# Kernel tuning notes

Measured on AMD Instinct MI355X. Metric: run time of the kernel, lower is better.

The kernel has to match this reference:

```python
import jax, jax.numpy as jnp
import numpy as np

B, N, DIM, H, DK, DV = 2, 2048, 1536, 8, 64, 192


def relative_shift(x):
    # x: [b, h, t1, 2*t1-1] -> [b, h, t1, t1] via Transformer-XL pad/reshape trick
    b, h, t1, t2 = x.shape
    x = jnp.pad(x, ((0, 0), (0, 0), (0, 0), (1, 0)))  # prepend zero column
    t2p = t2 + 1
    x = x.reshape(b, h, t2p, t1)
    x = x[:, :, 1:, :].reshape(b, h, t1, t2)
    return x[..., : (t2p + 1) // 2]


def setup_inputs() -> dict:
    key = jax.random.key(0)
    ks = jax.random.split(key, 9)
    s = 0.02
    return {
        "x": jax.random.normal(ks[0], (B, N, DIM), jnp.float32),
        "Wq": jax.random.normal(ks[1], (DIM, H * DK), jnp.float32) * s,
        "Wk": jax.random.normal(ks[2], (DIM, H * DK), jnp.float32) * s,
        "Wv": jax.random.normal(ks[3], (DIM, H * DV), jnp.float32) * s,
        "W_rel": jax.random.normal(ks[4], (1, H * DK), jnp.float32) * s,
        "Wo": jax.random.normal(ks[5], (H * DV, DIM), jnp.float32) * s,
        "bo": jnp.zeros((DIM,), jnp.float32),
        "rel_content_bias": jax.random.normal(ks[6], (1, H, 1, DK), jnp.float32),
        "rel_pos_bias": jax.random.normal(ks[7], (1, H, 1, DK), jnp.float32),
    }


def reference(x, Wq, Wk, Wv, W_rel, Wo, bo, rel_content_bias, rel_pos_bias):
    b, n, _ = x.shape
    scale = DK ** -0.5
    split = lambda t, d: t.reshape(b, n, H, d).transpose(0, 2, 1, 3)  # b h n d
    q = split(x @ Wq, DK) * scale
    k = split(x @ Wk, DK)
    v = split(x @ Wv, DV)

    content_logits = jnp.einsum("bhid,bhjd->bhij", q + rel_content_bias, k)

    distances = jnp.arange(-n + 1, n, dtype=jnp.float32)[:, None]  # [2n-1, 1]
    rel_k = (distances @ W_rel).reshape(2 * n - 1, H, DK).transpose(1, 0, 2)  # h j d
    rel_logits = jnp.einsum("bhid,hjd->bhij", q + rel_pos_bias, rel_k)
    rel_logits = relative_shift(rel_logits)

    attn = jax.nn.softmax(content_logits + rel_logits, axis=-1)
    out = jnp.einsum("bhij,bhjd->bhid", attn, v)
    out = out.transpose(0, 2, 1, 3).reshape(b, n, H * DV)
    return out @ Wo + bo
```

## Files before the change

kernel.cpp:

```cpp
#include <hip/hip_runtime.h>
#include <math.h>

typedef __attribute__((ext_vector_type(8))) short short8;
typedef __attribute__((ext_vector_type(4))) float floatx4;

namespace {
constexpr int kB = 2, kN = 2048, kDIM = 1536, kH = 8, kDK = 64, kDV = 192;
constexpr int kHDV = kH * kDV;
constexpr float kScale = 0.125f;
constexpr float kLog2e = 1.44269504088896340736f;
}

__device__ __forceinline__ unsigned short f2b(float f) {
    union { float f; unsigned u; } v; v.f = f;
    unsigned r = (v.u + 0x7FFFu + ((v.u >> 16) & 1u)) >> 16;
    return (unsigned short)r;
}
__device__ __forceinline__ unsigned short f2b_fast(float f) {
    union { float f; unsigned u; } v; v.f = f;
    return (unsigned short)((v.u + 0x8000u) >> 16);
}

__global__ __launch_bounds__(256) void conv_w(
    const float* __restrict__ src, unsigned short* __restrict__ dst, int Ncols)
{
    __shared__ float Ts[32][33];
    const int tx = threadIdx.x & 31, ty = threadIdx.x >> 5;
    const int k0 = blockIdx.x * 32, n0 = blockIdx.y * 32;
#pragma unroll
    for (int p = 0; p < 4; ++p)
        Ts[ty + p * 8][tx] = src[(size_t)(k0 + ty + p * 8) * Ncols + n0 + tx];
    __syncthreads();
#pragma unroll
    for (int p = 0; p < 4; ++p)
        dst[(size_t)(n0 + ty + p * 8) * kDIM + k0 + tx] = f2b(Ts[tx][ty + p * 8]);
}

__global__ __launch_bounds__(256) void conv_x(
    const float* __restrict__ x, unsigned short* __restrict__ xb)
{
    int idx = blockIdx.x * 256 + threadIdx.x;
    float4 v = *(const float4*)&x[(size_t)idx * 4];
    ushort4 o; o.x = f2b(v.x); o.y = f2b(v.y); o.z = f2b(v.z); o.w = f2b(v.w);
    *(ushort4*)&xb[(size_t)idx * 4] = o;
}

__global__ __launch_bounds__(256) void wcm_pre(
    const float* __restrict__ Wq, const float* __restrict__ Wrel,
    const float* __restrict__ rpb, float* __restrict__ wcm)
{
    int gid = blockIdx.x * 256 + threadIdx.x;
    if (gid < 12288) {
        int dim = gid >> 3, h = gid & 7;
        float s = 0.f;
#pragma unroll 8
        for (int d = 0; d < 64; ++d)
            s += Wq[(size_t)dim * 512 + h * 64 + d] * Wrel[h * 64 + d];
        wcm[h * kDIM + dim] = s * kScale * kLog2e;
    } else if (gid < 12296) {
        int h = gid - 12288;
        float s = 0.f;
#pragma unroll 8
        for (int d = 0; d < 64; ++d) s += rpb[h * 64 + d] * Wrel[h * 64 + d];
        wcm[12288 + h] = s * kLog2e;
    }
}

__global__ __launch_bounds__(256) void c_gemm(
    const float* __restrict__ x, const float* __restrict__ wcm,
    float* __restrict__ cw)
{
    const int row  = blockIdx.x * 4 + (threadIdx.x >> 6);
    const int lane = threadIdx.x & 63;
    const float* xr = x + (size_t)row * kDIM;

    float4 xv[6];
#pragma unroll
    for (int c = 0; c < 6; ++c)
        xv[c] = *(const float4*)&xr[c * 256 + lane * 4];

    float acc[8];
#pragma unroll
    for (int h = 0; h < 8; ++h) {
        const float* wr = wcm + h * kDIM;
        float a = 0.f;
#pragma unroll
        for (int c = 0; c < 6; ++c) {
            float4 wv = *(const float4*)&wr[c * 256 + lane * 4];
            a += xv[c].x * wv.x + xv[c].y * wv.y + xv[c].z * wv.z + xv[c].w * wv.w;
        }
        acc[h] = a;
    }
#pragma unroll
    for (int h = 0; h < 8; ++h) {
        float a = acc[h];
        a += __shfl_xor(a, 1, 64);
        a += __shfl_xor(a, 2, 64);
        a += __shfl_xor(a, 4, 64);
        a += __shfl_xor(a, 8, 64);
        a += __shfl_xor(a, 16, 64);
        a += __shfl_xor(a, 32, 64);
        acc[h] = a;
    }
    if (lane == 0) {
        const int b = row >> 11, i = row & 2047;
#pragma unroll
        for (int h = 0; h < 8; ++h)
            cw[(size_t)(b * 8 + h) * kN + i] = acc[h] + wcm[12288 + h];
    }
}

__global__ __launch_bounds__(256) void mm_qkv(
    const unsigned short* __restrict__ xb,
    const unsigned short* __restrict__ wt,
    const float* __restrict__ rcb,
    unsigned short* __restrict__ qo,
    unsigned short* __restrict__ ko,
    unsigned short* __restrict__ vo)
{
    __shared__ unsigned short A_lds[128 * 72];
    __shared__ unsigned short B_lds[128 * 72];
    const int tid = threadIdx.x;
    const int wave = tid >> 6, lane = tid & 63, lm = lane & 15, lg = lane >> 4;
    const int bm = blockIdx.y * 128, bn = blockIdx.x * 128;
    const int mb = (wave >> 1) * 64, nb = (wave & 1) * 64;

    floatx4 acc[4][4];
#pragma unroll
    for (int i = 0; i < 4; ++i)
#pragma unroll
        for (int j = 0; j < 4; ++j)
#pragma unroll
            for (int r = 0; r < 4; ++r) acc[i][j][r] = 0.f;

    const int srow = tid >> 3, scc = (tid & 7) * 8;
    short8 ra[4], rb[4];
#pragma unroll
    for (int p = 0; p < 4; ++p) {
        ra[p] = *(const short8*)&xb[(size_t)(bm + srow + p * 32) * kDIM + scc];
        rb[p] = *(const short8*)&wt[(size_t)(bn + srow + p * 32) * kDIM + scc];
    }

    for (int kt = 0; kt < 24; ++kt) {
        __syncthreads();
#pragma unroll
        for (int p = 0; p < 4; ++p) {
            *(short8*)&A_lds[(srow + p * 32) * 72 + scc] = ra[p];
            *(short8*)&B_lds[(srow + p * 32) * 72 + scc] = rb[p];
        }
        __syncthreads();
        if (kt < 23) {
            int k0 = (kt + 1) * 64;
#pragma unroll
            for (int p = 0; p < 4; ++p) {
                ra[p] = *(const short8*)&xb[(size_t)(bm + srow + p * 32) * kDIM + k0 + scc];
                rb[p] = *(const short8*)&wt[(size_t)(bn + srow + p * 32) * kDIM + k0 + scc];
            }
        }
#pragma unroll
        for (int ks = 0; ks < 2; ++ks) {
            short8 af[4], bf[4];
#pragma unroll
            for (int mi = 0; mi < 4; ++mi)
                af[mi] = *(const short8*)&A_lds[(mb + mi * 16 + lm) * 72 + lg * 8 + 32 * ks];
#pragma unroll
            for (int ni = 0; ni < 4; ++ni)
                bf[ni] = *(const short8*)&B_lds[(nb + ni * 16 + lm) * 72 + lg * 8 + 32 * ks];
#pragma unroll
            for (int mi = 0; mi < 4; ++mi)
#pragma unroll
                for (int ni = 0; ni < 4; ++ni)
                    acc[mi][ni] = __builtin_amdgcn_mfma_f32_16x16x32_bf16(
                        af[mi], bf[ni], acc[mi][ni], 0, 0, 0);
        }
    }

#pragma unroll
    for (int mi = 0; mi < 4; ++mi)
#pragma unroll
        for (int ni = 0; ni < 4; ++ni)
#pragma unroll
            for (int r = 0; r < 4; ++r) {
                int row = bm + mb + mi * 16 + lg * 4 + r;
                int b = row >> 11, i = row & 2047;
                int col = bn + nb + ni * 16 + lm;
                float v = acc[mi][ni][r];
                if (bn < 512) {
                    int h = col >> 6, d = col & 63;
                    qo[((size_t)(b * 8 + h) * kN + i) * kDK + d] =
                        f2b((v * kScale + rcb[h * 64 + d]) * kLog2e);
                } else if (bn < 1024) {
                    int c2 = col - 512, h = c2 >> 6, d = c2 & 63;
                    ko[((size_t)(b * 8 + h) * kN + i) * kDK + d] = f2b(v);
                } else {
                    int c2 = col - 1024, h = c2 / 192, d = c2 - h * 192;
                    vo[((size_t)(b * 8 + h) * kN + i) * kDV + d] = f2b(v);
                }
            }
}

__global__ __launch_bounds__(256) void vtrans(
    const unsigned short* __restrict__ vw, unsigned short* __restrict__ vt)
{
    __shared__ unsigned short Ts[32][33];
    const int tx = threadIdx.x & 31, ty = threadIdx.x >> 5;
    const int i0 = blockIdx.x * 32, d0 = blockIdx.y * 32, bh = blockIdx.z;
#pragma unroll
    for (int p = 0; p < 4; ++p)
        Ts[ty + p * 8][tx] = vw[((size_t)bh * kN + i0 + ty + p * 8) * kDV + d0 + tx];
    __syncthreads();
#pragma unroll
    for (int p = 0; p < 4; ++p)
        vt[((size_t)bh * kDV + d0 + ty + p * 8) * kN + i0 + tx] = Ts[tx][ty + p * 8];
}

__global__ __launch_bounds__(256) void flash_attn(
    const unsigned short* __restrict__ q,
    const unsigned short* __restrict__ k,
    const unsigned short* __restrict__ vt,
    const float* __restrict__ crel,
    unsigned short* __restrict__ ao)
{
    __shared__ unsigned short K_lds[64 * 72];
    __shared__ unsigned short V_lds[192 * 72];
    __shared__ unsigned short P_lds[4 * 16 * 68];

    const int tid = threadIdx.x;
    const int wave = tid >> 6, lane = tid & 63, lm = lane & 15, lg = lane >> 4;
    const int id = blockIdx.x;
    const int rem = id >> 3;
    const int bh = (id & 7) * 2 + (rem >> 5);
    const int i0 = (rem & 31) * 64;

    short8 qA[2];
    {
        const size_t qb = ((size_t)bh * kN + i0 + wave * 16 + lm) * kDK + lg * 8;
        qA[0] = *(const short8*)&q[qb];
        qA[1] = *(const short8*)&q[qb + 32];
    }
    float cR[4], gici[4];
#pragma unroll
    for (int r = 0; r < 4; ++r) {
        const int row = wave * 16 + lg * 4 + r;
        cR[r]   = crel[(size_t)bh * kN + i0 + row];
        gici[r] = (float)(i0 + row) * cR[r];
    }

    floatx4 o4[12];
#pragma unroll
    for (int nd = 0; nd < 12; ++nd)
#pragma unroll
        for (int r = 0; r < 4; ++r) o4[nd][r] = 0.f;
    floatx4 lacc;
#pragma unroll
    for (int r = 0; r < 4; ++r) lacc[r] = 0.f;
    float m_[4] = {-INFINITY, -INFINITY, -INFINITY, -INFINITY};

    const unsigned short* kb = k + (size_t)bh * kN * kDK;
    const unsigned short* vb = vt + (size_t)bh * kDV * kN;
    const int pbase = wave * 16 * 68;
    const int srow = tid >> 3, scol = (tid & 7) * 8;

    short8 ones;
#pragma unroll
    for (int u = 0; u < 8; ++u) ones[u] = (short)0x3F80;

    for (int t = 0; t < 32; ++t) {
        const int j0 = t * 64;
        __syncthreads();
#pragma unroll
        for (int p = 0; p < 2; ++p)
            *(short8*)&K_lds[(srow + p * 32) * 72 + scol] =
                *(const short8*)&kb[(size_t)(j0 + srow + p * 32) * kDK + scol];
#pragma unroll
        for (int p = 0; p < 6; ++p)
            *(short8*)&V_lds[(srow + p * 32) * 72 + scol] =
                *(const short8*)&vb[(size_t)(srow + p * 32) * kN + j0 + scol];
        __syncthreads();

        floatx4 s4[4];
#pragma unroll
        for (int st = 0; st < 4; ++st) {
#pragma unroll
            for (int r = 0; r < 4; ++r) s4[st][r] = 0.f;
#pragma unroll
            for (int ks = 0; ks < 2; ++ks) {
                short8 kf = *(const short8*)&K_lds[(st * 16 + lm) * 72 + lg * 8 + 32 * ks];
                s4[st] = __builtin_amdgcn_mfma_f32_16x16x32_bf16(qA[ks], kf, s4[st], 0, 0, 0);
            }
        }

        float sv[4][4];
        float lmax[4];
#pragma unroll
        for (int r = 0; r < 4; ++r) lmax[r] = -INFINITY;
#pragma unroll
        for (int st = 0; st < 4; ++st) {
            const float jf = (float)(j0 + st * 16 + lm);
#pragma unroll
            for (int r = 0; r < 4; ++r) {
                float v = fmaf(jf, cR[r], s4[st][r] - gici[r]);
                sv[st][r] = v;
                lmax[r] = fmaxf(lmax[r], v);
            }
        }
        bool ok = (lmax[0] <= m_[0] + 8.f) && (lmax[1] <= m_[1] + 8.f) &&
                  (lmax[2] <= m_[2] + 8.f) && (lmax[3] <= m_[3] + 8.f);
        if (!__all(ok)) {
#pragma unroll
            for (int r = 0; r < 4; ++r) {
                float mx = lmax[r];
                mx = fmaxf(mx, __shfl_xor(mx, 1, 64));
                mx = fmaxf(mx, __shfl_xor(mx, 2, 64));
                mx = fmaxf(mx, __shfl_xor(mx, 4, 64));
                mx = fmaxf(mx, __shfl_xor(mx, 8, 64));
                float mnew = fmaxf(m_[r], mx);
                float alpha = exp2f(m_[r] - mnew);
                m_[r] = mnew;
                lacc[r] *= alpha;
#pragma unroll
                for (int nd = 0; nd < 12; ++nd) o4[nd][r] *= alpha;
            }
        }
#pragma unroll
        for (int st = 0; st < 4; ++st)
#pragma unroll
            for (int r = 0; r < 4; ++r)
                P_lds[pbase + (lg * 4 + r) * 68 + st * 16 + lm] =
                    f2b_fast(exp2f(sv[st][r] - m_[r]));

        short8 pa[2];
        pa[0] = *(const short8*)&P_lds[pbase + lm * 68 + lg * 8];
        pa[1] = *(const short8*)&P_lds[pbase + lm * 68 + lg * 8 + 32];
        lacc = __builtin_amdgcn_mfma_f32_16x16x32_bf16(pa[0], ones, lacc, 0, 0, 0);
        lacc = __builtin_amdgcn_mfma_f32_16x16x32_bf16(pa[1], ones, lacc, 0, 0, 0);
#pragma unroll
        for (int nd = 0; nd < 12; ++nd) {
#pragma unroll
            for (int ks = 0; ks < 2; ++ks) {
                short8 vf = *(const short8*)&V_lds[(nd * 16 + lm) * 72 + lg * 8 + 32 * ks];
                o4[nd] = __builtin_amdgcn_mfma_f32_16x16x32_bf16(pa[ks], vf, o4[nd], 0, 0, 0);
            }
        }
    }

    const int b = bh >> 3, h = bh & 7;
#pragma unroll
    for (int r = 0; r < 4; ++r) {
        float inv = 1.f / lacc[r];
        size_t rowbase = ((size_t)b * kN + i0 + wave * 16 + lg * 4 + r) * (size_t)kHDV
                         + h * kDV;
#pragma unroll
        for (int nd = 0; nd < 12; ++nd)
            ao[rowbase + nd * 16 + lm] = f2b(o4[nd][r] * inv);
    }
}

__global__ __launch_bounds__(256) void mm_out(
    const unsigned short* __restrict__ aw,
    const unsigned short* __restrict__ wot,
    const float* __restrict__ bias,
    float* __restrict__ out)
{
    __shared__ unsigned short A_lds[128 * 72];
    __shared__ unsigned short B_lds[128 * 72];
    const int tid = threadIdx.x;
    const int wave = tid >> 6, lane = tid & 63, lm = lane & 15, lg = lane >> 4;
    const int bm = blockIdx.y * 128, bn = blockIdx.x * 128;
    const int mb = (wave >> 1) * 64, nb = (wave & 1) * 64;

    floatx4 acc[4][4];
#pragma unroll
    for (int i = 0; i < 4; ++i)
#pragma unroll
        for (int j = 0; j < 4; ++j)
#pragma unroll
            for (int r = 0; r < 4; ++r) acc[i][j][r] = 0.f;

    const int srow = tid >> 3, scc = (tid & 7) * 8;
    short8 ra[4], rb[4];
#pragma unroll
    for (int p = 0; p < 4; ++p) {
        ra[p] = *(const short8*)&aw[(size_t)(bm + srow + p * 32) * kDIM + scc];
        rb[p] = *(const short8*)&wot[(size_t)(bn + srow + p * 32) * kDIM + scc];
    }

    for (int kt = 0; kt < 24; ++kt) {
        __syncthreads();
#pragma unroll
        for (int p = 0; p < 4; ++p) {
            *(short8*)&A_lds[(srow + p * 32) * 72 + scc] = ra[p];
            *(short8*)&B_lds[(srow + p * 32) * 72 + scc] = rb[p];
        }
        __syncthreads();
        if (kt < 23) {
            int k0 = (kt + 1) * 64;
#pragma unroll
            for (int p = 0; p < 4; ++p) {
                ra[p] = *(const short8*)&aw[(size_t)(bm + srow + p * 32) * kDIM + k0 + scc];
                rb[p] = *(const short8*)&wot[(size_t)(bn + srow + p * 32) * kDIM + k0 + scc];
            }
        }
#pragma unroll
        for (int ks = 0; ks < 2; ++ks) {
            short8 af[4], bf[4];
#pragma unroll
            for (int mi = 0; mi < 4; ++mi)
                af[mi] = *(const short8*)&A_lds[(mb + mi * 16 + lm) * 72 + lg * 8 + 32 * ks];
#pragma unroll
            for (int ni = 0; ni < 4; ++ni)
                bf[ni] = *(const short8*)&B_lds[(nb + ni * 16 + lm) * 72 + lg * 8 + 32 * ks];
#pragma unroll
            for (int mi = 0; mi < 4; ++mi)
#pragma unroll
                for (int ni = 0; ni < 4; ++ni)
                    acc[mi][ni] = __builtin_amdgcn_mfma_f32_16x16x32_bf16(
                        af[mi], bf[ni], acc[mi][ni], 0, 0, 0);
        }
    }

#pragma unroll
    for (int mi = 0; mi < 4; ++mi)
#pragma unroll
        for (int ni = 0; ni < 4; ++ni)
#pragma unroll
            for (int r = 0; r < 4; ++r) {
                int row = bm + mb + mi * 16 + lg * 4 + r;
                int col = bn + nb + ni * 16 + lm;
                out[(size_t)row * kDIM + col] = acc[mi][ni][r] + bias[col];
            }
}

extern "C" void kernel_launch(void* const* d_in, const int* in_sizes, int n_in,
                              void* d_out, int out_size, void* d_ws, size_t ws_size,
                              hipStream_t stream)
{
    const float* x    = (const float*)d_in[0];
    const float* Wq   = (const float*)d_in[1];
    const float* Wk   = (const float*)d_in[2];
    const float* Wv   = (const float*)d_in[3];
    const float* Wrel = (const float*)d_in[4];
    const float* Wo   = (const float*)d_in[5];
    const float* bo   = (const float*)d_in[6];
    const float* rcb  = (const float*)d_in[7];
    const float* rpb  = (const float*)d_in[8];
    float* out = (float*)d_out;

    char* w = (char*)d_ws;
    unsigned short* xb  = (unsigned short*)(w);
    unsigned short* wt  = (unsigned short*)(w + 12582912);
    unsigned short* qw  = (unsigned short*)(w + 20447232);
    unsigned short* kw  = (unsigned short*)(w + 24641536);
    unsigned short* vw  = (unsigned short*)(w + 28835840);
    float*          cw  = (float*)(w + 41418752);
    float*          wcm = (float*)(w + 41549824);
    unsigned short* vtp = xb;
    unsigned short* awp = vw;
    unsigned short* wot = wt;

    { dim3 g(48, 16);  conv_w<<<g, 256, 0, stream>>>(Wq, wt,               512); }
    { dim3 g(48, 16);  conv_w<<<g, 256, 0, stream>>>(Wk, wt + 512  * 1536, 512); }
    { dim3 g(48, 48);  conv_w<<<g, 256, 0, stream>>>(Wv, wt + 1024 * 1536, 1536); }
    conv_x<<<6144, 256, 0, stream>>>(x, xb);
    wcm_pre<<<49, 256, 0, stream>>>(Wq, Wrel, rpb, wcm);
    c_gemm<<<1024, 256, 0, stream>>>(x, wcm, cw);

    { dim3 g(20, 32); mm_qkv<<<g, 256, 0, stream>>>(xb, wt, rcb, qw, kw, vw); }

    { dim3 g(48, 48); conv_w<<<g, 256, 0, stream>>>(Wo, wot, 1536); }
    { dim3 g(64, 6, 16); vtrans<<<g, 256, 0, stream>>>(vw, vtp); }

    flash_attn<<<512, 256, 0, stream>>>(qw, kw, vtp, cw, awp);

    { dim3 g(12, 32); mm_out<<<g, 256, 0, stream>>>(awp, wot, bo, out); }
}
```

Before: 329.4 us.

## Batch weight conversions, fuse x cast into c_gemm, use global_load_lds in GEMMs

Merges the four weight transpose/convert launches into one grid-z kernel and folds the x-to-bf16 cast into the relative-bias row-dot kernel, cutting launches and one extra read of x. The QKV and output GEMMs now load tiles straight into LDS with global_load_lds instead of staging through registers with padded LDS rows. The GEMMs lose their register prefetch, so global loads no longer overlap the MFMA work, and the unpadded 64-wide LDS rows may add bank conflicts on fragment reads. The workspace is relaid so the Wo buffer no longer aliases wt.

```diff
diff --git a/kernel.cpp b/kernel.cpp
--- a/kernel.cpp
+++ b/kernel.cpp
@@ -20,13 +20,28 @@
     union { float f; unsigned u; } v; v.f = f;
     return (unsigned short)((v.u + 0x8000u) >> 16);
 }
-
-__global__ __launch_bounds__(256) void conv_w(
-    const float* __restrict__ src, unsigned short* __restrict__ dst, int Ncols)
-{
+__device__ __forceinline__ void gl16(const void* g, void* l) {
+    __builtin_amdgcn_global_load_lds(
+        (const __attribute__((address_space(1))) unsigned int*)g,
+        (__attribute__((address_space(3))) unsigned int*)l, 16, 0, 0);
+}
+
+__global__ __launch_bounds__(256) void convw_all(
+    const float* __restrict__ Wq, const float* __restrict__ Wk,
+    const float* __restrict__ Wv, const float* __restrict__ Wo,
+    unsigned short* __restrict__ wt, unsigned short* __restrict__ wot)
+{
+    const int z = blockIdx.z;
+    const float* src; unsigned short* dst; int Ncols;
+    if (z == 0)      { src = Wq; dst = wt;               Ncols = 512; }
+    else if (z == 1) { src = Wk; dst = wt + 512 * kDIM;  Ncols = 512; }
+    else if (z == 2) { src = Wv; dst = wt + 1024 * kDIM; Ncols = 1536; }
+    else             { src = Wo; dst = wot;              Ncols = 1536; }
+    const int n0 = blockIdx.y * 32;
+    if (n0 >= Ncols) return;
     __shared__ float Ts[32][33];
     const int tx = threadIdx.x & 31, ty = threadIdx.x >> 5;
-    const int k0 = blockIdx.x * 32, n0 = blockIdx.y * 32;
+    const int k0 = blockIdx.x * 32;
 #pragma unroll
     for (int p = 0; p < 4; ++p)
         Ts[ty + p * 8][tx] = src[(size_t)(k0 + ty + p * 8) * Ncols + n0 + tx];
@@ -34,15 +49,6 @@
 #pragma unroll
     for (int p = 0; p < 4; ++p)
         dst[(size_t)(n0 + ty + p * 8) * kDIM + k0 + tx] = f2b(Ts[tx][ty + p * 8]);
-}
-
-__global__ __launch_bounds__(256) void conv_x(
-    const float* __restrict__ x, unsigned short* __restrict__ xb)
-{
-    int idx = blockIdx.x * 256 + threadIdx.x;
-    float4 v = *(const float4*)&x[(size_t)idx * 4];
-    ushort4 o; o.x = f2b(v.x); o.y = f2b(v.y); o.z = f2b(v.z); o.w = f2b(v.w);
-    *(ushort4*)&xb[(size_t)idx * 4] = o;
 }
 
 __global__ __launch_bounds__(256) void wcm_pre(
@@ -66,9 +72,9 @@
     }
 }
 
-__global__ __launch_bounds__(256) void c_gemm(
+__global__ __launch_bounds__(256) void xc_fused(
     const float* __restrict__ x, const float* __restrict__ wcm,
-    float* __restrict__ cw)
+    unsigned short* __restrict__ xb, float* __restrict__ cw)
 {
     const int row  = blockIdx.x * 4 + (threadIdx.x >> 6);
     const int lane = threadIdx.x & 63;
@@ -78,6 +84,14 @@
 #pragma unroll
     for (int c = 0; c < 6; ++c)
         xv[c] = *(const float4*)&xr[c * 256 + lane * 4];
+
+#pragma unroll
+    for (int c = 0; c < 6; ++c) {
+        ushort4 o;
+        o.x = f2b(xv[c].x); o.y = f2b(xv[c].y);
+        o.z = f2b(xv[c].z); o.w = f2b(xv[c].w);
+        *(ushort4*)&xb[(size_t)row * kDIM + c * 256 + lane * 4] = o;
+    }
 
     float acc[8];
 #pragma unroll
@@ -118,13 +132,18 @@
     unsigned short* __restrict__ ko,
     unsigned short* __restrict__ vo)
 {
-    __shared__ unsigned short A_lds[128 * 72];
-    __shared__ unsigned short B_lds[128 * 72];
+    __shared__ unsigned short A_l[128 * 64];
+    __shared__ unsigned short B_l[128 * 64];
     const int tid = threadIdx.x;
     const int wave = tid >> 6, lane = tid & 63, lm = lane & 15, lg = lane >> 4;
     const int bm = blockIdx.y * 128, bn = blockIdx.x * 128;
     const int mb = (wave >> 1) * 64, nb = (wave & 1) * 64;
 
+    const int r0 = tid >> 3, c0 = (tid & 7) * 8;
+    const unsigned short* pa = xb + (size_t)(bm + r0) * kDIM + c0;
+    const unsigned short* pb = wt + (size_t)(bn + r0) * kDIM + c0;
+    const int ldst = wave * 512;
+
     floatx4 acc[4][4];
 #pragma unroll
     for (int i = 0; i < 4; ++i)
@@ -133,39 +152,24 @@
 #pragma unroll
             for (int r = 0; r < 4; ++r) acc[i][j][r] = 0.f;
 
-    const int srow = tid >> 3, scc = (tid & 7) * 8;
-    short8 ra[4], rb[4];
-#pragma unroll
-    for (int p = 0; p < 4; ++p) {
-        ra[p] = *(const short8*)&xb[(size_t)(bm + srow + p * 32) * kDIM + scc];
-        rb[p] = *(const short8*)&wt[(size_t)(bn + srow + p * 32) * kDIM + scc];
-    }
-
     for (int kt = 0; kt < 24; ++kt) {
-        __syncthreads();
-#pragma unroll
-        for (int p = 0; p < 4; ++p) {
-            *(short8*)&A_lds[(srow + p * 32) * 72 + scc] = ra[p];
-            *(short8*)&B_lds[(srow + p * 32) * 72 + scc] = rb[p];
-        }
-        __syncthreads();
-        if (kt < 23) {
-            int k0 = (kt + 1) * 64;
-#pragma unroll
-            for (int p = 0; p < 4; ++p) {
-                ra[p] = *(const short8*)&xb[(size_t)(bm + srow + p * 32) * kDIM + k0 + scc];
-                rb[p] = *(const short8*)&wt[(size_t)(bn + srow + p * 32) * kDIM + k0 + scc];
-            }
-        }
+        const int k0 = kt * 64;
+        __syncthreads();
+#pragma unroll
+        for (int i = 0; i < 4; ++i) {
+            gl16(pa + (size_t)i * 32 * kDIM + k0, &A_l[i * 2048 + ldst]);
+            gl16(pb + (size_t)i * 32 * kDIM + k0, &B_l[i * 2048 + ldst]);
+        }
+        __syncthreads();
 #pragma unroll
         for (int ks = 0; ks < 2; ++ks) {
             short8 af[4], bf[4];
 #pragma unroll
             for (int mi = 0; mi < 4; ++mi)
-                af[mi] = *(const short8*)&A_lds[(mb + mi * 16 + lm) * 72 + lg * 8 + 32 * ks];
+                af[mi] = *(const short8*)&A_l[(mb + mi * 16 + lm) * 64 + lg * 8 + 32 * ks];
 #pragma unroll
             for (int ni = 0; ni < 4; ++ni)
-                bf[ni] = *(const short8*)&B_lds[(nb + ni * 16 + lm) * 72 + lg * 8 + 32 * ks];
+                bf[ni] = *(const short8*)&B_l[(nb + ni * 16 + lm) * 64 + lg * 8 + 32 * ks];
 #pragma unroll
             for (int mi = 0; mi < 4; ++mi)
 #pragma unroll
@@ -362,13 +366,18 @@
     const float* __restrict__ bias,
     float* __restrict__ out)
 {
-    __shared__ unsigned short A_lds[128 * 72];
-    __shared__ unsigned short B_lds[128 * 72];
+    __shared__ unsigned short A_l[128 * 64];
+    __shared__ unsigned short B_l[128 * 64];
     const int tid = threadIdx.x;
     const int wave = tid >> 6, lane = tid & 63, lm = lane & 15, lg = lane >> 4;
     const int bm = blockIdx.y * 128, bn = blockIdx.x * 128;
     const int mb = (wave >> 1) * 64, nb = (wave & 1) * 64;
 
+    const int r0 = tid >> 3, c0 = (tid & 7) * 8;
+    const unsigned short* pa = aw + (size_t)(bm + r0) * kDIM + c0;
+    const unsigned short* pb = wot + (size_t)(bn + r0) * kDIM + c0;
+    const int ldst = wave * 512;
+
     floatx4 acc[4][4];
 #pragma unroll
     for (int i = 0; i < 4; ++i)
@@ -377,39 +386,24 @@
 #pragma unroll
             for (int r = 0; r < 4; ++r) acc[i][j][r] = 0.f;
 
-    const int srow = tid >> 3, scc = (tid & 7) * 8;
-    short8 ra[4], rb[4];
-#pragma unroll
-    for (int p = 0; p < 4; ++p) {
-        ra[p] = *(const short8*)&aw[(size_t)(bm + srow + p * 32) * kDIM + scc];
-        rb[p] = *(const short8*)&wot[(size_t)(bn + srow + p * 32) * kDIM + scc];
-    }
-
     for (int kt = 0; kt < 24; ++kt) {
-        __syncthreads();
-#pragma unroll
-        for (int p = 0; p < 4; ++p) {
-            *(short8*)&A_lds[(srow + p * 32) * 72 + scc] = ra[p];
-            *(short8*)&B_lds[(srow + p * 32) * 72 + scc] = rb[p];
-        }
-        __syncthreads();
-        if (kt < 23) {
-            int k0 = (kt + 1) * 64;
-#pragma unroll
-            for (int p = 0; p < 4; ++p) {
-                ra[p] = *(const short8*)&aw[(size_t)(bm + srow + p * 32) * kDIM + k0 + scc];
-                rb[p] = *(const short8*)&wot[(size_t)(bn + srow + p * 32) * kDIM + k0 + scc];
-            }
-        }
+        const int k0 = kt * 64;
+        __syncthreads();
+#pragma unroll
+        for (int i = 0; i < 4; ++i) {
+            gl16(pa + (size_t)i * 32 * kDIM + k0, &A_l[i * 2048 + ldst]);
+            gl16(pb + (size_t)i * 32 * kDIM + k0, &B_l[i * 2048 + ldst]);
+        }
+        __syncthreads();
 #pragma unroll
         for (int ks = 0; ks < 2; ++ks) {
             short8 af[4], bf[4];
 #pragma unroll
             for (int mi = 0; mi < 4; ++mi)
-                af[mi] = *(const short8*)&A_lds[(mb + mi * 16 + lm) * 72 + lg * 8 + 32 * ks];
+                af[mi] = *(const short8*)&A_l[(mb + mi * 16 + lm) * 64 + lg * 8 + 32 * ks];
 #pragma unroll
             for (int ni = 0; ni < 4; ++ni)
-                bf[ni] = *(const short8*)&B_lds[(nb + ni * 16 + lm) * 72 + lg * 8 + 32 * ks];
+                bf[ni] = *(const short8*)&B_l[(nb + ni * 16 + lm) * 64 + lg * 8 + 32 * ks];
 #pragma unroll
             for (int mi = 0; mi < 4; ++mi)
 #pragma unroll
@@ -449,25 +443,21 @@
     char* w = (char*)d_ws;
     unsigned short* xb  = (unsigned short*)(w);
     unsigned short* wt  = (unsigned short*)(w + 12582912);
-    unsigned short* qw  = (unsigned short*)(w + 20447232);
-    unsigned short* kw  = (unsigned short*)(w + 24641536);
-    unsigned short* vw  = (unsigned short*)(w + 28835840);
-    float*          cw  = (float*)(w + 41418752);
-    float*          wcm = (float*)(w + 41549824);
+    unsigned short* wot = (unsigned short*)(w + 20447232);
+    unsigned short* qw  = (unsigned short*)(w + 25165824);
+    unsigned short* kw  = (unsigned short*)(w + 29360128);
+    unsigned short* vw  = (unsigned short*)(w + 33554432);
+    float*          cw  = (float*)(w + 46137344);
+    float*          wcm = (float*)(w + 46268416);
     unsigned short* vtp = xb;
     unsigned short* awp = vw;
-    unsigned short* wot = wt;
-
-    { dim3 g(48, 16);  conv_w<<<g, 256, 0, stream>>>(Wq, wt,               512); }
-    { dim3 g(48, 16);  conv_w<<<g, 256, 0, stream>>>(Wk, wt + 512  * 1536, 512); }
-    { dim3 g(48, 48);  conv_w<<<g, 256, 0, stream>>>(Wv, wt + 1024 * 1536, 1536); }
-    conv_x<<<6144, 256, 0, stream>>>(x, xb);
+
     wcm_pre<<<49, 256, 0, stream>>>(Wq, Wrel, rpb, wcm);
-    c_gemm<<<1024, 256, 0, stream>>>(x, wcm, cw);
+    { dim3 g(48, 48, 4); convw_all<<<g, 256, 0, stream>>>(Wq, Wk, Wv, Wo, wt, wot); }
+    xc_fused<<<1024, 256, 0, stream>>>(x, wcm, xb, cw);
 
     { dim3 g(20, 32); mm_qkv<<<g, 256, 0, stream>>>(xb, wt, rcb, qw, kw, vw); }
 
-    { dim3 g(48, 48); conv_w<<<g, 256, 0, stream>>>(Wo, wot, 1536); }
     { dim3 g(64, 6, 16); vtrans<<<g, 256, 0, stream>>>(vw, vtp); }
 
     flash_attn<<<512, 256, 0, stream>>>(qw, kw, vtp, cw, awp);
```

After: 339.7 us. 1.03x slower.
